# Optimization experiments

Measured on AMD Instinct MI355X. Metric: run time of the kernel, lower is better.

## Reference

```python
import jax, jax.numpy as jnp
import numpy as np

B, S, D, H = 2, 2048, 1280, 16
DEPTH = D // H  # 80


def setup_inputs() -> dict:
    key = jax.random.key(0)
    ks = jax.random.split(key, 6)
    scale = 1.0 / np.sqrt(D)
    x = jax.random.normal(ks[0], (B, S, D), dtype=jnp.float32)
    # causal mask: 1.0 where attention is disallowed (strict upper triangle)
    mask = jnp.triu(jnp.ones((S, S), dtype=jnp.float32), k=1)
    Wq = jax.random.normal(ks[1], (D, D), dtype=jnp.float32) * scale
    Wk = jax.random.normal(ks[2], (D, D), dtype=jnp.float32) * scale
    Wv = jax.random.normal(ks[3], (D, D), dtype=jnp.float32) * scale
    Wo = jax.random.normal(ks[4], (D, D), dtype=jnp.float32) * scale
    z = jnp.zeros((D,), dtype=jnp.float32)
    return {"x": x, "mask": mask, "Wq": Wq, "bq": z, "Wk": Wk, "bk": z,
            "Wv": Wv, "bv": z, "Wo": Wo, "bo": z}


def _split_heads(t):
    # [B, S, D] -> [B, H, S, depth]
    return t.reshape(B, -1, H, DEPTH).transpose(0, 2, 1, 3)


def reference(x, mask, Wq, bq, Wk, bk, Wv, bv, Wo, bo):
    q = _split_heads(x @ Wq + bq)
    k = _split_heads(x @ Wk + bk)
    v = _split_heads(x @ Wv + bv)
    # scaled dot-product attention with additive (masked * -10000) logits
    logits = jnp.einsum("bhqd,bhkd->bhqk", q, k) / jnp.sqrt(
        jnp.asarray(DEPTH, dtype=jnp.float32))
    logits = logits + mask * -10000.0  # mask broadcasts over [B, H]
    attn = jax.nn.softmax(logits, axis=-1)
    ctx = jnp.einsum("bhqk,bhkd->bhqd", attn, v)
    ctx = ctx.transpose(0, 2, 1, 3).reshape(B, -1, D)  # merge heads
    return ctx @ Wo + bo
```

## Files before the change

### kernel.cpp

```cpp
#include <hip/hip_runtime.h>

typedef unsigned short u16;
typedef __bf16 bf16;
typedef __bf16 bf16x8 __attribute__((ext_vector_type(8)));
typedef unsigned short u16x8 __attribute__((ext_vector_type(8)));
typedef float f32x4 __attribute__((ext_vector_type(4)));

constexpr int B_ = 2, S_ = 2048, D_ = 1280, H_ = 16, DEPTH_ = 80;
constexpr int M_ = B_ * S_;
constexpr int QR_ = 128;

__device__ inline u16 f2b(float f) { return __builtin_bit_cast(u16, (bf16)f); }

typedef __attribute__((address_space(1))) const void gvoid;
typedef __attribute__((address_space(3))) void lvoid;
__device__ inline void gl_lds16(const void* g, void* l) {
  __builtin_amdgcn_global_load_lds((gvoid*)g, (lvoid*)l, 16, 0, 0);
}

__global__ __launch_bounds__(256) void convx_k(const float* __restrict__ src,
                                               u16* __restrict__ dst) {
  int i0 = (blockIdx.x * 256 + threadIdx.x) * 8;
  u16x8 v;
#pragma unroll
  for (int j = 0; j < 8; ++j) v[j] = f2b(src[i0 + j]);
  *(u16x8*)(dst + i0) = v;
}

__global__ __launch_bounds__(256) void transpose4_k(const float* W0, const float* W1,
                                                    const float* W2, const float* W3,
                                                    u16* __restrict__ WT) {
  const float* srcs[4] = {W0, W1, W2, W3};
  const float* W = srcs[blockIdx.z];
  u16* out = WT + (size_t)blockIdx.z * D_ * D_;
  __shared__ u16 t[32][33];
  int tx = threadIdx.x, ty = threadIdx.y;
  int x0 = blockIdx.x * 32, y0 = blockIdx.y * 32;
#pragma unroll
  for (int i = 0; i < 4; ++i)
    t[ty + 8 * i][tx] = f2b(W[(size_t)(y0 + ty + 8 * i) * D_ + x0 + tx]);
  __syncthreads();
#pragma unroll
  for (int i = 0; i < 4; ++i)
    out[(size_t)(x0 + ty + 8 * i) * D_ + y0 + tx] = t[tx][ty + 8 * i];
}

struct GemmAcc {
  f32x4 acc[4][4];
};
__device__ inline void gemm_core(const u16* __restrict__ A,
                                 const u16* __restrict__ BT, int m0, int n0,
                                 u16* a_s, u16* b_s, GemmAcc& g) {
  int tid = threadIdx.x, lane = tid & 63, wave = tid >> 6;
  int quad = lane >> 4, l15 = lane & 15;
  int wm = wave >> 1, wn = wave & 1;
  int rr8 = lane >> 3;
  int csw = ((lane & 7) ^ rr8) * 8;
  int sw15 = l15 & 7;

  for (int k0 = 0; k0 < D_; k0 += 64) {
    __syncthreads();
#pragma unroll
    for (int j = 0; j < 4; ++j) {
      int ch = wave * 4 + j;
      gl_lds16(A + (size_t)(m0 + ch * 8 + rr8) * D_ + k0 + csw, a_s + ch * 512);
      gl_lds16(BT + (size_t)(n0 + ch * 8 + rr8) * D_ + k0 + csw, b_s + ch * 512);
    }
    __syncthreads();
#pragma unroll
    for (int ks = 0; ks < 2; ++ks) {
      int pos = (((ks << 2) | quad) ^ sw15) * 8;
      bf16x8 af[4], bfr[4];
#pragma unroll
      for (int mt = 0; mt < 4; ++mt)
        af[mt] = *(const bf16x8*)(a_s + (wm * 64 + mt * 16 + l15) * 64 + pos);
#pragma unroll
      for (int nt = 0; nt < 4; ++nt)
        bfr[nt] = *(const bf16x8*)(b_s + (wn * 64 + nt * 16 + l15) * 64 + pos);
#pragma unroll
      for (int mt = 0; mt < 4; ++mt)
#pragma unroll
        for (int nt = 0; nt < 4; ++nt)
          g.acc[mt][nt] = __builtin_amdgcn_mfma_f32_16x16x32_bf16(
              af[mt], bfr[nt], g.acc[mt][nt], 0, 0, 0);
    }
  }
}

__global__ __launch_bounds__(256) void gemm_qkv(const u16* __restrict__ A,
                                                const u16* __restrict__ BT,
                                                const float* __restrict__ bq,
                                                const float* __restrict__ bk,
                                                const float* __restrict__ bv,
                                                u16* __restrict__ Qw,
                                                u16* __restrict__ Kw,
                                                u16* __restrict__ Vw) {
  __shared__ __align__(16) u16 a_s[128 * 64];
  __shared__ __align__(16) u16 b_s[128 * 64];
  int lane = threadIdx.x & 63, wave = threadIdx.x >> 6;
  int quad = lane >> 4, l15 = lane & 15;
  int wm = wave >> 1, wn = wave & 1;
  int m0 = blockIdx.y * 128, n0 = blockIdx.x * 128;

  GemmAcc g = {};
  gemm_core(A, BT, m0, n0, a_s, b_s, g);

  int mat = n0 / D_;
  const float* bp = (mat == 0) ? bq : (mat == 1 ? bk : bv);
#pragma unroll
  for (int nt = 0; nt < 4; ++nt) {
    int ng = n0 + wn * 64 + nt * 16 + l15;
    int co = ng - mat * D_;
    float bv_ = bp[co];
    int h = co / DEPTH_, d = co % DEPTH_;
#pragma unroll
    for (int mt = 0; mt < 4; ++mt)
#pragma unroll
      for (int r = 0; r < 4; ++r) {
        int row = m0 + wm * 64 + mt * 16 + quad * 4 + r;
        int b = row >> 11, s = row & (S_ - 1);
        u16 bits = f2b(g.acc[mt][nt][r] + bv_);
        if (mat < 2) {
          u16* outp = mat ? Kw : Qw;
          outp[((size_t)(b * H_ + h) * S_ + s) * QR_ + d] = bits;
        } else {
          Vw[((size_t)(b * H_ + h) * DEPTH_ + d) * S_ + s] = bits;
        }
      }
  }
}

__global__ __launch_bounds__(256) void gemm_out(const u16* __restrict__ A,
                                                const u16* __restrict__ BT,
                                                const float* __restrict__ bias,
                                                float* __restrict__ out) {
  __shared__ __align__(16) u16 a_s[128 * 64];
  __shared__ __align__(16) u16 b_s[128 * 64];
  int lane = threadIdx.x & 63, wave = threadIdx.x >> 6;
  int quad = lane >> 4, l15 = lane & 15;
  int wm = wave >> 1, wn = wave & 1;
  int m0 = blockIdx.y * 128, n0 = blockIdx.x * 128;

  GemmAcc g = {};
  gemm_core(A, BT, m0, n0, a_s, b_s, g);

#pragma unroll
  for (int nt = 0; nt < 4; ++nt) {
    int col = n0 + wn * 64 + nt * 16 + l15;
    float bv = bias[col];
#pragma unroll
    for (int mt = 0; mt < 4; ++mt)
#pragma unroll
      for (int r = 0; r < 4; ++r) {
        int row = m0 + wm * 64 + mt * 16 + quad * 4 + r;
        out[(size_t)row * D_ + col] = g.acc[mt][nt][r] + bv;
      }
  }
}

__global__ __launch_bounds__(256) void attn_k(const u16* __restrict__ Qp,
                                              const u16* __restrict__ Kp,
                                              const u16* __restrict__ VT,
                                              u16* __restrict__ ctx) {
  constexpr float SCALE = 0.11180339887498949f;
  __shared__ __align__(16) u16 q_s[128 * 128];
  __shared__ __align__(16) u16 k_s[64 * 128];
  __shared__ __align__(16) u16 vt_s[80 * 64];
  __shared__ __align__(16) u16 p_s[64 * 72];
  int tid = threadIdx.x, lane = tid & 63, wave = tid >> 6;
  int quad = lane >> 4, l15 = lane & 15;
  int pi = blockIdx.x, bh = blockIdx.y;
  int tlo = pi, thi = 31 - pi;
  const u16* Qb = Qp + (size_t)bh * S_ * QR_;
  const u16* Kb = Kp + (size_t)bh * S_ * QR_;
  const u16* Vb = VT + (size_t)bh * DEPTH_ * S_;

#pragma unroll
  for (int i = 0; i < 8; ++i) {
    int row = wave * 4 + quad + 16 * i;
    int gr = (row < 64) ? (tlo * 64 + row) : (thi * 64 + row - 64);
    int sc = l15 ^ (row & 7);
    gl_lds16(Qb + (size_t)gr * QR_ + sc * 8, q_s + (size_t)row * QR_ + l15 * 8);
  }

  f32x4 o_lo[5] = {}, o_hi[5] = {};
  float l_lo[4] = {}, l_hi[4] = {};

  auto tile_step = [&](int qrow0, bool diag, f32x4* acc_o, float* lsum) {
    f32x4 sa[4] = {};
#pragma unroll
    for (int ks = 0; ks < 3; ++ks) {
      int pa = ((ks * 4 + quad) ^ (l15 & 7)) * 8;
      bf16x8 af = *(const bf16x8*)(q_s + (size_t)(qrow0 + wave * 16 + l15) * QR_ + pa);
#pragma unroll
      for (int nt = 0; nt < 4; ++nt) {
        bf16x8 bfr = *(const bf16x8*)(k_s + (size_t)(nt * 16 + l15) * QR_ + pa);
        sa[nt] = __builtin_amdgcn_mfma_f32_16x16x32_bf16(af, bfr, sa[nt], 0, 0, 0);
      }
    }
#pragma unroll
    for (int nt = 0; nt < 4; ++nt)
#pragma unroll
      for (int r = 0; r < 4; ++r) {
        float p = __expf(sa[nt][r] * SCALE);
        if (diag && (nt * 16 + l15) > (wave * 16 + quad * 4 + r)) p = 0.0f;
        sa[nt][r] = p;
        lsum[r] += p;
      }
    asm volatile("s_waitcnt lgkmcnt(0)" ::: "memory");
#pragma unroll
    for (int nt = 0; nt < 4; ++nt)
#pragma unroll
      for (int r = 0; r < 4; ++r)
        p_s[(wave * 16 + quad * 4 + r) * 72 + nt * 16 + l15] = f2b(sa[nt][r]);
    asm volatile("s_waitcnt lgkmcnt(0)" ::: "memory");
#pragma unroll
    for (int kk = 0; kk < 2; ++kk) {
      bf16x8 af = *(const bf16x8*)(p_s + (wave * 16 + l15) * 72 + kk * 32 + quad * 8);
#pragma unroll
      for (int d5 = 0; d5 < 5; ++d5) {
        int pv = ((kk * 4 + quad) ^ (l15 & 7)) * 8;
        bf16x8 bfr = *(const bf16x8*)(vt_s + (size_t)(d5 * 16 + l15) * 64 + pv);
        acc_o[d5] = __builtin_amdgcn_mfma_f32_16x16x32_bf16(af, bfr, acc_o[d5], 0, 0, 0);
      }
    }
  };

  for (int kt = 0; kt <= thi; ++kt) {
    int k0 = kt * 64;
    __syncthreads();
#pragma unroll
    for (int i = 0; i < 4; ++i) {
      int row = wave * 4 + quad + 16 * i;
      int sc = l15 ^ (row & 7);
      gl_lds16(Kb + (size_t)(k0 + row) * QR_ + sc * 8,
               k_s + (size_t)row * QR_ + l15 * 8);
    }
#pragma unroll
    for (int i = 0; i < 3; ++i) {
      int ch = tid + 256 * i;
      if (ch < 640) {
        int row = ch >> 3, pos = ch & 7;
        int sc = pos ^ (row & 7);
        gl_lds16(Vb + (size_t)row * S_ + k0 + sc * 8, vt_s + ch * 8);
      }
    }
    __syncthreads();
    tile_step(64, kt == thi, o_hi, l_hi);
    if (kt <= tlo) tile_step(0, kt == tlo, o_lo, l_lo);
  }

#pragma unroll
  for (int r = 0; r < 4; ++r) {
#pragma unroll
    for (int m = 1; m < 16; m <<= 1) {
      l_lo[r] += __shfl_xor(l_lo[r], m, 16);
      l_hi[r] += __shfl_xor(l_hi[r], m, 16);
    }
  }

  int b = bh >> 4, h = bh & 15;
#pragma unroll
  for (int d5 = 0; d5 < 5; ++d5)
#pragma unroll
    for (int r = 0; r < 4; ++r) {
      int rl = wave * 16 + quad * 4 + r;
      int col = h * DEPTH_ + d5 * 16 + l15;
      ctx[(size_t)(b * S_ + tlo * 64 + rl) * D_ + col] = f2b(o_lo[d5][r] / l_lo[r]);
      ctx[(size_t)(b * S_ + thi * 64 + rl) * D_ + col] = f2b(o_hi[d5][r] / l_hi[r]);
    }
}

extern "C" void kernel_launch(void* const* d_in, const int* in_sizes, int n_in,
                              void* d_out, int out_size, void* d_ws, size_t ws_size,
                              hipStream_t stream) {
  const float* x  = (const float*)d_in[0];
  const float* Wq = (const float*)d_in[2];
  const float* bq = (const float*)d_in[3];
  const float* Wk = (const float*)d_in[4];
  const float* bk = (const float*)d_in[5];
  const float* Wv = (const float*)d_in[6];
  const float* bv = (const float*)d_in[7];
  const float* Wo = (const float*)d_in[8];
  const float* bo = (const float*)d_in[9];

  const size_t DD = (size_t)D_ * D_;
  const size_t QE = (size_t)B_ * H_ * S_ * DEPTH_;
  const size_t QP = (size_t)B_ * H_ * S_ * QR_;
  u16* xbf = (u16*)d_ws;
  u16* wT  = xbf + QE;
  u16* Qw  = wT + 4 * DD;
  u16* Kw  = Qw + QP;
  u16* Vw  = Kw + QP;
  u16* Cw  = xbf;
  size_t need = (size_t)(Vw + QE - xbf) * 2;
  if (ws_size < need) return;

  hipMemsetAsync(Qw, 0, 2 * QP * sizeof(u16), stream);
  convx_k<<<(int)(QE / 2048), 256, 0, stream>>>(x, xbf);
  transpose4_k<<<dim3(D_ / 32, D_ / 32, 4), dim3(32, 8), 0, stream>>>(Wq, Wk, Wv,
                                                                      Wo, wT);
  gemm_qkv<<<dim3(3 * D_ / 128, M_ / 128), 256, 0, stream>>>(xbf, wT, bq, bk, bv,
                                                             Qw, Kw, Vw);
  attn_k<<<dim3(16, B_ * H_), 256, 0, stream>>>(Qw, Kw, Vw, Cw);
  gemm_out<<<dim3(D_ / 128, M_ / 128), 256, 0, stream>>>(Cw, wT + 3 * DD, bo,
                                                         (float*)d_out);
}
```

Baseline: 285.9 us.

## Split attention into single Q-tile blocks with register Q and zero only padding

The attention kernel now processes one 64-row query tile per block and keeps the Q fragments in registers instead of a paired lo/hi tile staged in LDS. This doubles the grid, lowers LDS use per block and sets a min-blocks launch bound to raise occupancy. The full memset of the padded Q/K buffers is replaced by a small kernel that zeroes only the 48 padding columns per row. The cost is relying on the scheduler for causal load balance instead of explicit tile pairing, plus one extra kernel launch.

After: 276.1 us. -3.5%, faster.

```diff
diff --git a/kernel.cpp b/kernel.cpp
--- a/kernel.cpp
+++ b/kernel.cpp
@@ -25,6 +25,13 @@
 #pragma unroll
   for (int j = 0; j < 8; ++j) v[j] = f2b(src[i0 + j]);
   *(u16x8*)(dst + i0) = v;
+}
+
+__global__ __launch_bounds__(256) void pad0_k(u16* __restrict__ QK) {
+  int c = blockIdx.x * 256 + threadIdx.x;
+  int r = c / 6, k = c - r * 6;
+  u16x8 z = {};
+  *(u16x8*)(QK + (size_t)r * QR_ + 80 + k * 8) = z;
 }
 
 __global__ __launch_bounds__(256) void transpose4_k(const float* W0, const float* W1,
@@ -158,75 +165,34 @@
   }
 }
 
-__global__ __launch_bounds__(256) void attn_k(const u16* __restrict__ Qp,
-                                              const u16* __restrict__ Kp,
-                                              const u16* __restrict__ VT,
-                                              u16* __restrict__ ctx) {
+__global__ __launch_bounds__(256, 4) void attn_k(const u16* __restrict__ Qp,
+                                                 const u16* __restrict__ Kp,
+                                                 const u16* __restrict__ VT,
+                                                 u16* __restrict__ ctx) {
   constexpr float SCALE = 0.11180339887498949f;
-  __shared__ __align__(16) u16 q_s[128 * 128];
   __shared__ __align__(16) u16 k_s[64 * 128];
   __shared__ __align__(16) u16 vt_s[80 * 64];
   __shared__ __align__(16) u16 p_s[64 * 72];
   int tid = threadIdx.x, lane = tid & 63, wave = tid >> 6;
   int quad = lane >> 4, l15 = lane & 15;
-  int pi = blockIdx.x, bh = blockIdx.y;
-  int tlo = pi, thi = 31 - pi;
+  int bx = blockIdx.x, by = blockIdx.y;
+  int s_ = (by >> 4) & 1;
+  int qt = s_ ? (31 - bx) : bx;
+  int bh = (by & 15) | (((by >> 5) & 1) << 4);
   const u16* Qb = Qp + (size_t)bh * S_ * QR_;
   const u16* Kb = Kp + (size_t)bh * S_ * QR_;
   const u16* Vb = VT + (size_t)bh * DEPTH_ * S_;
 
-#pragma unroll
-  for (int i = 0; i < 8; ++i) {
-    int row = wave * 4 + quad + 16 * i;
-    int gr = (row < 64) ? (tlo * 64 + row) : (thi * 64 + row - 64);
-    int sc = l15 ^ (row & 7);
-    gl_lds16(Qb + (size_t)gr * QR_ + sc * 8, q_s + (size_t)row * QR_ + l15 * 8);
-  }
-
-  f32x4 o_lo[5] = {}, o_hi[5] = {};
-  float l_lo[4] = {}, l_hi[4] = {};
-
-  auto tile_step = [&](int qrow0, bool diag, f32x4* acc_o, float* lsum) {
-    f32x4 sa[4] = {};
-#pragma unroll
-    for (int ks = 0; ks < 3; ++ks) {
-      int pa = ((ks * 4 + quad) ^ (l15 & 7)) * 8;
-      bf16x8 af = *(const bf16x8*)(q_s + (size_t)(qrow0 + wave * 16 + l15) * QR_ + pa);
-#pragma unroll
-      for (int nt = 0; nt < 4; ++nt) {
-        bf16x8 bfr = *(const bf16x8*)(k_s + (size_t)(nt * 16 + l15) * QR_ + pa);
-        sa[nt] = __builtin_amdgcn_mfma_f32_16x16x32_bf16(af, bfr, sa[nt], 0, 0, 0);
-      }
-    }
-#pragma unroll
-    for (int nt = 0; nt < 4; ++nt)
-#pragma unroll
-      for (int r = 0; r < 4; ++r) {
-        float p = __expf(sa[nt][r] * SCALE);
-        if (diag && (nt * 16 + l15) > (wave * 16 + quad * 4 + r)) p = 0.0f;
-        sa[nt][r] = p;
-        lsum[r] += p;
-      }
-    asm volatile("s_waitcnt lgkmcnt(0)" ::: "memory");
-#pragma unroll
-    for (int nt = 0; nt < 4; ++nt)
-#pragma unroll
-      for (int r = 0; r < 4; ++r)
-        p_s[(wave * 16 + quad * 4 + r) * 72 + nt * 16 + l15] = f2b(sa[nt][r]);
-    asm volatile("s_waitcnt lgkmcnt(0)" ::: "memory");
-#pragma unroll
-    for (int kk = 0; kk < 2; ++kk) {
-      bf16x8 af = *(const bf16x8*)(p_s + (wave * 16 + l15) * 72 + kk * 32 + quad * 8);
-#pragma unroll
-      for (int d5 = 0; d5 < 5; ++d5) {
-        int pv = ((kk * 4 + quad) ^ (l15 & 7)) * 8;
-        bf16x8 bfr = *(const bf16x8*)(vt_s + (size_t)(d5 * 16 + l15) * 64 + pv);
-        acc_o[d5] = __builtin_amdgcn_mfma_f32_16x16x32_bf16(af, bfr, acc_o[d5], 0, 0, 0);
-      }
-    }
-  };
-
-  for (int kt = 0; kt <= thi; ++kt) {
+  bf16x8 qf[3];
+#pragma unroll
+  for (int ks = 0; ks < 3; ++ks)
+    qf[ks] = *(const bf16x8*)(Qb + (size_t)(qt * 64 + wave * 16 + l15) * QR_ +
+                              ks * 32 + quad * 8);
+
+  f32x4 acc_o[5] = {};
+  float lsum[4] = {};
+
+  for (int kt = 0; kt <= qt; ++kt) {
     int k0 = kt * 64;
     __syncthreads();
 #pragma unroll
@@ -246,28 +212,59 @@
       }
     }
     __syncthreads();
-    tile_step(64, kt == thi, o_hi, l_hi);
-    if (kt <= tlo) tile_step(0, kt == tlo, o_lo, l_lo);
+
+    f32x4 sa[4] = {};
+#pragma unroll
+    for (int ks = 0; ks < 3; ++ks) {
+      int pa = ((ks * 4 + quad) ^ (l15 & 7)) * 8;
+#pragma unroll
+      for (int nt = 0; nt < 4; ++nt) {
+        bf16x8 bfr = *(const bf16x8*)(k_s + (size_t)(nt * 16 + l15) * QR_ + pa);
+        sa[nt] = __builtin_amdgcn_mfma_f32_16x16x32_bf16(qf[ks], bfr, sa[nt], 0, 0, 0);
+      }
+    }
+    bool diag = (kt == qt);
+#pragma unroll
+    for (int nt = 0; nt < 4; ++nt)
+#pragma unroll
+      for (int r = 0; r < 4; ++r) {
+        float p = __expf(sa[nt][r] * SCALE);
+        if (diag && (nt * 16 + l15) > (wave * 16 + quad * 4 + r)) p = 0.0f;
+        sa[nt][r] = p;
+        lsum[r] += p;
+      }
+    asm volatile("s_waitcnt lgkmcnt(0)" ::: "memory");
+#pragma unroll
+    for (int nt = 0; nt < 4; ++nt)
+#pragma unroll
+      for (int r = 0; r < 4; ++r)
+        p_s[(wave * 16 + quad * 4 + r) * 72 + nt * 16 + l15] = f2b(sa[nt][r]);
+    asm volatile("s_waitcnt lgkmcnt(0)" ::: "memory");
+#pragma unroll
+    for (int kk = 0; kk < 2; ++kk) {
+      bf16x8 af = *(const bf16x8*)(p_s + (wave * 16 + l15) * 72 + kk * 32 + quad * 8);
+#pragma unroll
+      for (int d5 = 0; d5 < 5; ++d5) {
+        int pv = ((kk * 4 + quad) ^ (l15 & 7)) * 8;
+        bf16x8 bfr = *(const bf16x8*)(vt_s + (size_t)(d5 * 16 + l15) * 64 + pv);
+        acc_o[d5] = __builtin_amdgcn_mfma_f32_16x16x32_bf16(af, bfr, acc_o[d5], 0, 0, 0);
+      }
+    }
   }
 
 #pragma unroll
-  for (int r = 0; r < 4; ++r) {
-#pragma unroll
-    for (int m = 1; m < 16; m <<= 1) {
-      l_lo[r] += __shfl_xor(l_lo[r], m, 16);
-      l_hi[r] += __shfl_xor(l_hi[r], m, 16);
-    }
-  }
+  for (int r = 0; r < 4; ++r)
+#pragma unroll
+    for (int m = 1; m < 16; m <<= 1) lsum[r] += __shfl_xor(lsum[r], m, 16);
 
   int b = bh >> 4, h = bh & 15;
 #pragma unroll
   for (int d5 = 0; d5 < 5; ++d5)
 #pragma unroll
     for (int r = 0; r < 4; ++r) {
-      int rl = wave * 16 + quad * 4 + r;
+      int s = qt * 64 + wave * 16 + quad * 4 + r;
       int col = h * DEPTH_ + d5 * 16 + l15;
-      ctx[(size_t)(b * S_ + tlo * 64 + rl) * D_ + col] = f2b(o_lo[d5][r] / l_lo[r]);
-      ctx[(size_t)(b * S_ + thi * 64 + rl) * D_ + col] = f2b(o_hi[d5][r] / l_hi[r]);
+      ctx[(size_t)(b * S_ + s) * D_ + col] = f2b(acc_o[d5][r] / lsum[r]);
     }
 }
 
@@ -296,13 +293,13 @@
   size_t need = (size_t)(Vw + QE - xbf) * 2;
   if (ws_size < need) return;
 
-  hipMemsetAsync(Qw, 0, 2 * QP * sizeof(u16), stream);
   convx_k<<<(int)(QE / 2048), 256, 0, stream>>>(x, xbf);
+  pad0_k<<<3072, 256, 0, stream>>>(Qw);
   transpose4_k<<<dim3(D_ / 32, D_ / 32, 4), dim3(32, 8), 0, stream>>>(Wq, Wk, Wv,
                                                                       Wo, wT);
   gemm_qkv<<<dim3(3 * D_ / 128, M_ / 128), 256, 0, stream>>>(xbf, wT, bq, bk, bv,
                                                              Qw, Kw, Vw);
-  attn_k<<<dim3(16, B_ * H_), 256, 0, stream>>>(Qw, Kw, Vw, Cw);
+  attn_k<<<dim3(16, 64), 256, 0, stream>>>(Qw, Kw, Vw, Cw);
   gemm_out<<<dim3(D_ / 128, M_ / 128), 256, 0, stream>>>(Cw, wT + 3 * DD, bo,
                                                          (float*)d_out);
 }
```
